# Optimization experiments

Measured on AMD Instinct MI355X. Metric: run time of the kernel, lower is better.

Reference implementation:

```python
import jax, jax.numpy as jnp
import numpy as np

# WAGE-style quantizer (NeuroSim training path): round to 2^(b-1) levels, clip to (-1+1/S, 1-1/S),
# straight-through estimator for gradients.

def wage_q(x, bits=8):
    S = 2.0 ** (bits - 1)
    q = jnp.clip(jnp.round(x * S) / S, -1.0 + 1.0 / S, 1.0 - 1.0 / S)
    return x + jax.lax.stop_gradient(q - x)


def qconv(x, w, stride, pad, wl_w=8, wl_a=8):
    wq = wage_q(w, wl_w)
    y = jax.lax.conv_general_dilated(
        x, wq, window_strides=(stride, stride),
        padding=[(pad, pad), (pad, pad)],
        dimension_numbers=('NCHW', 'OIHW', 'NCHW'))
    return wage_q(y, wl_a)


def pad_hw(x, p):
    return jnp.pad(x, ((0, 0), (0, 0), (p, p), (p, p)))


def crop_like(x, tgt):
    return x[:, :, :tgt.shape[2], :tgt.shape[3]]


WEIGHT_SHAPES = {
    'w1': (64, 4, 3, 3), 'w2': (128, 64, 3, 3), 'w3': (256, 128, 3, 3), 'w4': (512, 256, 3, 3),
    'wr11': (512, 512, 3, 3), 'wr12': (512, 512, 3, 3), 'wr21': (512, 512, 3, 3), 'wr22': (512, 512, 3, 3),
    'wd3': (128, 512, 4, 4), 'wd2': (64, 416, 4, 4), 'wd1': (4, 224, 4, 4),
    'wu43': (32, 512, 4, 4), 'wu32': (32, 416, 4, 4), 'wu21': (32, 224, 4, 4), 'wu10': (32, 100, 4, 4),
    'wfc': (1, 32),
}


def setup_inputs() -> dict:
    key = jax.random.key(0)
    keys = jax.random.split(key, len(WEIGHT_SHAPES) + 1)
    inp = {'x': jax.random.normal(keys[0], (8, 4, 256, 256), dtype=jnp.float32)}
    for i, (name, shp) in enumerate(WEIGHT_SHAPES.items()):
        fan_in = int(np.prod(shp[1:]))
        inp[name] = jax.random.normal(keys[i + 1], shp, dtype=jnp.float32) / np.sqrt(fan_in)
    return inp


def reference(x, w1, w2, w3, w4, wr11, wr12, wr21, wr22,
              wd3, wd2, wd1, wu43, wu32, wu21, wu10, wfc):
    c1 = qconv(x, w1, 2, 1)        # [B,64,128,128]
    c2 = qconv(c1, w2, 2, 1)       # [B,128,64,64]
    c3 = qconv(c2, w3, 2, 1)       # [B,256,32,32]
    c4 = qconv(c3, w4, 2, 1)       # [B,512,16,16]
    r11 = qconv(c4, wr11, 1, 1)
    r12 = (1.0 - qconv(r11, wr12, 1, 1)) * c4
    r21 = qconv(r12, wr21, 1, 1)
    r22 = (1.0 - qconv(r21, wr22, 1, 1)) * r12
    r22p = pad_hw(r22, 8)                                   # [B,512,32,32]
    flow4_up = crop_like(qconv(r22p, wu43, 1, 2), c3)       # [B,32,32,32]
    d3 = crop_like(qconv(r22p, wd3, 1, 2), c3)              # [B,128,32,32]
    cat3 = pad_hw(jnp.concatenate([c3, d3, flow4_up], 1), 16)  # [B,416,64,64]
    flow3_up = crop_like(qconv(cat3, wu32, 1, 2), c2)
    d2 = crop_like(qconv(cat3, wd2, 1, 2), c2)
    cat2 = pad_hw(jnp.concatenate([c2, d2, flow3_up], 1), 32)  # [B,224,128,128]
    flow2_up = crop_like(qconv(cat2, wu21, 1, 2), c1)
    d1 = crop_like(qconv(cat2, wd1, 1, 2), c1)
    cat1 = pad_hw(jnp.concatenate([c1, d1, flow2_up], 1), 64)  # [B,100,256,256]
    u10 = qconv(cat1, wu10, 1, 2)                              # [B,32,257,257]
    feat = jnp.max(u10, axis=(2, 3))                           # AdaptiveMaxPool2d((1,1))
    out = wage_q(feat @ wage_q(wfc, 8).T, 8)                   # QLinear 32->1
    return out
```

## Files before the change

kernel.cpp:

```cpp
#include <hip/hip_runtime.h>

#define DEV __device__ __forceinline__

typedef __attribute__((ext_vector_type(4))) int i32x4;

DEV int wqi(float y) {
    int q = (int)rintf(y * 128.0f);
    return q < -127 ? -127 : (q > 127 ? 127 : q);
}
DEV unsigned encf(float f) { unsigned u = __float_as_uint(f); return (u & 0x80000000u) ? ~u : (u | 0x80000000u); }
DEV float decf(unsigned u) { return (u & 0x80000000u) ? __uint_as_float(u ^ 0x80000000u) : __uint_as_float(~u); }
DEV float wq8f(float x) {
    float q = rintf(x * 128.0f) * 0.0078125f;
    return fminf(fmaxf(q, -0.9921875f), 0.9921875f);
}

#define GLOAD16(g, l) __builtin_amdgcn_global_load_lds( \
    (const __attribute__((address_space(1))) void*)(g), \
    (__attribute__((address_space(3))) void*)(l), 16, 0, 0)

struct PackDesc {
    const float* w0; const float* w1; uint4* dst;
    int OC0, OC1, CinW, K, noct, nch64u, ndup;
};
struct PackArgs { PackDesc d[11]; int bofs[12]; };

__global__ void __launch_bounds__(256) k_packall(PackArgs a) {
    __shared__ unsigned char sb[16 * (64 * 16 + 4)];
    const int b = blockIdx.x;
    int i = 0;
    #pragma unroll
    for (int j = 1; j < 11; ++j) if (b >= a.bofs[j]) i = j;
    const PackDesc D = a.d[i];
    const int b2 = b - a.bofs[i];
    const int oct = b2 % D.noct;
    const int ch64u = b2 / D.noct;
    const int K2 = D.K * D.K;
    const int row_elems = 64 * K2;
    const int SSTR = row_elems + 4;
    const int QR = row_elems / 4;
    const int NQ = 16 * QR;
    const int cin0 = ch64u * 64;
    const int tid = threadIdx.x;

    for (int q = tid; q < NQ; q += 256) {
        const int r = q / QR, j = q - r * QR;
        const int oc = oct * 16 + r;
        const float* src = nullptr; int oci = 0;
        if (oc < D.OC0) { src = D.w0; oci = oc; }
        else if (oc < D.OC0 + D.OC1) { src = D.w1; oci = oc - D.OC0; }
        const int e0 = j * 4;
        float v[4] = {0.f, 0.f, 0.f, 0.f};
        if (src != nullptr) {
            const float* p = src + ((size_t)oci * D.CinW + cin0) * K2 + e0;
            const int cin_last = cin0 + (e0 + 3) / K2;
            if (cin_last < D.CinW) {
                const float4 f4 = *(const float4*)p;
                v[0] = f4.x; v[1] = f4.y; v[2] = f4.z; v[3] = f4.w;
            } else {
                #pragma unroll
                for (int e = 0; e < 4; ++e) {
                    const int cin = cin0 + (e0 + e) / K2;
                    if (cin < D.CinW) v[e] = p[e];
                }
            }
        }
        unsigned pk = 0;
        #pragma unroll
        for (int e = 0; e < 4; ++e) pk |= ((unsigned)(wqi(v[e]) & 255)) << (e * 8);
        *(unsigned*)&sb[r * SSTR + e0] = pk;
    }
    __syncthreads();

    const int outN = K2 * 64;
    for (int idx = tid; idx < outN; idx += 256) {
        const int kpos = idx >> 6, lane = idx & 63;
        const int l15 = lane & 15, g = lane >> 4;
        unsigned wd[4] = {0u, 0u, 0u, 0u};
        #pragma unroll
        for (int e = 0; e < 16; ++e) {
            const unsigned bval = sb[l15 * SSTR + (g * 16 + e) * K2 + kpos];
            wd[e >> 2] |= bval << ((e & 3) * 8);
        }
        uint4 u; u.x = wd[0]; u.y = wd[1]; u.z = wd[2]; u.w = wd[3];
        for (int d = 0; d < D.ndup; ++d) {
            const int ch64 = ch64u + d * D.nch64u;
            D.dst[((size_t)(ch64 * K2 + kpos) * D.noct + oct) * 64 + lane] = u;
        }
    }
}

__global__ void __launch_bounds__(256) k_conv1(const float* __restrict__ x, const float* __restrict__ w1,
                                               signed char* __restrict__ cat1) {
    __shared__ float sw2[36][64];
    __shared__ float sin_[4][17][17];
    const int tid = threadIdx.x;
    const int n = blockIdx.y;
    const int oh0 = (blockIdx.x >> 4) * 8, ow0 = (blockIdx.x & 15) * 8;
    for (int i = tid; i < 2304; i += 256) sw2[i % 36][i / 36] = wq8f(w1[i]);
    const int ih0 = oh0 * 2 - 1, iw0 = ow0 * 2 - 1;
    for (int i = tid; i < 4 * 289; i += 256) {
        const int c = i / 289, rem = i % 289, r = rem / 17, cc = rem % 17;
        const int ih = ih0 + r, iw = iw0 + cc;
        float v = 0.f;
        if ((unsigned)ih < 256u && (unsigned)iw < 256u) v = x[((size_t)(n * 4 + c) * 256 + ih) * 256 + iw];
        sin_[c][r][cc] = v;
    }
    __syncthreads();
    const int sp = tid & 63, ocg = tid >> 6;
    const int oh = sp >> 3, ow = sp & 7;
    float acc[16];
    #pragma unroll
    for (int j = 0; j < 16; ++j) acc[j] = 0.f;
    #pragma unroll
    for (int c = 0; c < 4; ++c)
    #pragma unroll
    for (int kh = 0; kh < 3; ++kh)
    #pragma unroll
    for (int kw = 0; kw < 3; ++kw) {
        const float v = sin_[c][oh * 2 + kh][ow * 2 + kw];
        const float4* wp4 = (const float4*)&sw2[c * 9 + kh * 3 + kw][ocg * 16];
        #pragma unroll
        for (int q = 0; q < 4; ++q) {
            const float4 wv = wp4[q];
            acc[q * 4 + 0] = fmaf(v, wv.x, acc[q * 4 + 0]);
            acc[q * 4 + 1] = fmaf(v, wv.y, acc[q * 4 + 1]);
            acc[q * 4 + 2] = fmaf(v, wv.z, acc[q * 4 + 2]);
            acc[q * 4 + 3] = fmaf(v, wv.w, acc[q * 4 + 3]);
        }
    }
    const size_t pix = ((size_t)(n * 128) + oh0 + oh) * 128 + ow0 + ow;
    unsigned wd[4] = {0u, 0u, 0u, 0u};
    #pragma unroll
    for (int j = 0; j < 16; ++j)
        wd[j >> 2] |= ((unsigned)(wqi(acc[j]) & 255)) << ((j & 3) * 8);
    uint4 u; u.x = wd[0]; u.y = wd[1]; u.z = wd[2]; u.w = wd[3];
    *(uint4*)(cat1 + pix * 112 + ocg * 16) = u;
}

__global__ void k_init(unsigned* __restrict__ feat, uint4* __restrict__ zbuf) {
    feat[threadIdx.x] = encf(-2.0f);
    if (threadIdx.x < 64) { uint4 z; z.x = z.y = z.z = z.w = 0u; zbuf[threadIdx.x] = z; }
}

__global__ void k_fc(const unsigned* __restrict__ feat, const float* __restrict__ wfc,
                     float* __restrict__ out) {
    int n = threadIdx.x;
    if (n < 8) {
        float s = 0.f;
        for (int c = 0; c < 32; ++c) s += decf(feat[n * 32 + c]) * wq8f(wfc[c]);
        out[n] = wq8f(s);
    }
}

__global__ void __launch_bounds__(256) k_comb(const int* __restrict__ ps, int nsl, int radix,
                                              int NP, int OC, double inv,
                                              signed char* __restrict__ dst, int dstr, int dch) {
    const int t = blockIdx.x * 256 + threadIdx.x;
    const int total = NP * (OC / 4);
    if (t >= total) return;
    const int opc = OC / 4;
    const int pix = t / opc, oc0 = (t - pix * opc) * 4;
    const size_t base = (size_t)pix * OC + oc0;
    const size_t NPOC = (size_t)NP * OC;
    long v0 = 0, v1 = 0, v2 = 0, v3 = 0;
    for (int s = 0; s < nsl; ++s) {
        const int4 p = *(const int4*)(ps + s * NPOC + base);
        v0 = v0 * radix + p.x; v1 = v1 * radix + p.y;
        v2 = v2 * radix + p.z; v3 = v3 * radix + p.w;
    }
    unsigned pk = 0;
    pk |= (unsigned)(wqi((float)((double)v0 * inv)) & 255);
    pk |= (unsigned)(wqi((float)((double)v1 * inv)) & 255) << 8;
    pk |= (unsigned)(wqi((float)((double)v2 * inv)) & 255) << 16;
    pk |= (unsigned)(wqi((float)((double)v3 * inv)) & 255) << 24;
    *(unsigned*)(dst + (size_t)pix * dstr + dch + oc0) = pk;
}

template<int K, int STR, int WM, int WN, int BN, int NBUF, int MODE, int RESF, int NSLICE, int NCHPS>
__global__ void __launch_bounds__(256) k_mconv(
    const signed char* __restrict__ s0, int Ctot, int st0,
    int S, int padeff,
    const uint4* __restrict__ wqp, int noct,
    signed char* __restrict__ dst, int dstr, int dch,
    signed char* __restrict__ dhl, int dhlstr, short* __restrict__ dj,
    const void* __restrict__ res, int rstr,
    unsigned* __restrict__ feat, int* __restrict__ ps,
    const signed char* __restrict__ zbuf,
    int OCv, int OH, int OW, int TILES_W, int nch,
    int NT, int NOCG, int swzq, int ORD)
{
    constexpr int TH = WM * 4;
    constexpr int RH = (TH - 1) * STR + K, RW = 7 * STR + K;
    constexpr int UPPS = 5;
    constexpr int K2 = K * K;
    constexpr int NUS = RH * RW * UPPS;
    constexpr int ROUNDS = (NUS + 255) / 256;
    constexpr int NUPS = ROUNDS * 256;
    constexpr int AHEAD = NBUF - 1;
    __shared__ uint4 lds[NBUF * NUPS];
    __shared__ float sred[4][2][16];

    const int tid = threadIdx.x, lane = tid & 63, w = tid >> 6;
    const int wm = w % WM, wn = w / WM;
    const int l15 = lane & 15, g = lane >> 4;

    const int b = blockIdx.x;
    const int work = (b & 7) * swzq + (b >> 3);
    int tile, n, ocg, slice;
    if (ORD == 0) {
        ocg = work % NOCG; const int t2 = work / NOCG;
        tile = t2 % NT; const int t3 = t2 / NT;
        n = t3 & 7; slice = t3 >> 3;
    } else {
        tile = work % NT; const int t2 = work / NT;
        n = t2 & 7; const int t3 = t2 >> 3;
        ocg = t3 % NOCG; slice = t3 / NOCG;
    }
    const int cin_off = slice * nch * 64;
    const uint4* wqpS = wqp + (size_t)slice * nch * K2 * noct * 64;

    const int tileh = tile / TILES_W, tilew = tile % TILES_W;
    const int oh0 = tileh * TH, ow0 = tilew * 8;
    const int ih0 = oh0 * STR - padeff, iw0 = ow0 * STR - padeff;
    const int blk_oct0 = ocg * (WN * BN);

    int pixb[2];
    #pragma unroll
    for (int am = 0; am < 2; ++am) {
        const int sp = wm * 32 + am * 16 + l15;
        pixb[am] = ((sp >> 3) * STR) * RW + (sp & 7) * STR;
    }

    i32x4 acc[2][BN];
    #pragma unroll
    for (int am = 0; am < 2; ++am)
        #pragma unroll
        for (int bn = 0; bn < BN; ++bn) acc[am][bn] = (i32x4){0, 0, 0, 0};
    long acc64[(NSLICE > 1) ? 2 * BN * 4 : 1];
    #pragma unroll
    for (int q = 0; q < ((NSLICE > 1) ? 2 * BN * 4 : 1); ++q) acc64[q] = 0;

    auto issue = [&](int ch, int buf) {
        uint4* lb = &lds[buf * NUPS];
        #pragma unroll
        for (int rd = 0; rd < ROUNDS; ++rd) {
            const int d = rd * 256 + tid;
            const signed char* gp = zbuf;
            if (d < NUS) {
                const int pix = d / UPPS;
                const int u = d - pix * UPPS;
                const int r = pix / RW, c = pix - r * RW;
                const int ih = ih0 + r, iw = iw0 + c;
                const int cin = cin_off + ch * 64 + u * 16;
                if (u < 4 && (unsigned)ih < (unsigned)S && (unsigned)iw < (unsigned)S && cin < Ctot)
                    gp = s0 + (((size_t)n * S + ih) * S + iw) * st0 + cin;
            }
            GLOAD16(gp, lb + rd * 256 + (tid & ~63));
        }
    };

    #pragma unroll
    for (int i = 0; i < AHEAD; ++i) if (i < nch) issue(i, i % NBUF);

    for (int ch = 0; ch < nch; ++ch) {
        if (ch + AHEAD < nch) issue(ch + AHEAD, (ch + AHEAD) % NBUF);
        const int infl = (nch - 1 - ch < AHEAD) ? nch - 1 - ch : AHEAD;
        if (infl >= 2)      __builtin_amdgcn_s_waitcnt(0xF70 | (2 * ROUNDS));
        else if (infl == 1) __builtin_amdgcn_s_waitcnt(0xF70 | ROUNDS);
        else                __builtin_amdgcn_s_waitcnt(0xF70);
        __builtin_amdgcn_s_barrier();
        __builtin_amdgcn_sched_barrier(0);
        const int bufo = (ch % NBUF) * NUPS;
        const int pb0 = bufo + pixb[0] * UPPS + g;
        const int pb1 = bufo + pixb[1] * UPPS + g;
        const size_t wbase = ((size_t)ch * K2 * noct + blk_oct0 + wn * BN) * 64 + lane;
        #pragma unroll
        for (int kpos = 0; kpos < K2; ++kpos) {
            const int kh = kpos / K, kw = kpos % K;
            const int po = (kh * RW + kw) * UPPS;
            i32x4 bfr[BN];
            #pragma unroll
            for (int bn = 0; bn < BN; ++bn) {
                union { uint4 u; i32x4 v; } bu;
                bu.u = wqpS[wbase + ((size_t)kpos * noct + bn) * 64];
                bfr[bn] = bu.v;
            }
            union { uint4 u; i32x4 v; } a0, a1;
            a0.u = lds[pb0 + po];
            a1.u = lds[pb1 + po];
            #pragma unroll
            for (int bn = 0; bn < BN; ++bn) {
                acc[0][bn] = __builtin_amdgcn_mfma_i32_16x16x64_i8(a0.v, bfr[bn], acc[0][bn], 0, 0, 0);
                acc[1][bn] = __builtin_amdgcn_mfma_i32_16x16x64_i8(a1.v, bfr[bn], acc[1][bn], 0, 0, 0);
            }
        }
        if constexpr (NSLICE > 1) {
            if (((ch + 1) & (NCHPS - 1)) == 0) {
                #pragma unroll
                for (int am = 0; am < 2; ++am)
                #pragma unroll
                for (int bn = 0; bn < BN; ++bn) {
                    #pragma unroll
                    for (int rg = 0; rg < 4; ++rg) {
                        acc64[(am * BN + bn) * 4 + rg] = acc64[(am * BN + bn) * 4 + rg] * 256 + (long)acc[am][bn][rg];
                    }
                    acc[am][bn] = (i32x4){0, 0, 0, 0};
                }
            }
        }
        __builtin_amdgcn_sched_barrier(0);
        __builtin_amdgcn_s_barrier();
    }

    if constexpr (MODE == 2) {
        #pragma unroll
        for (int bn = 0; bn < BN; ++bn) {
            float m = -2.0f;
            #pragma unroll
            for (int am = 0; am < 2; ++am)
                #pragma unroll
                for (int rg = 0; rg < 4; ++rg) {
                    const int sp = wm * 32 + am * 16 + g * 4 + rg;
                    const int oh = oh0 + (sp >> 3), ow = ow0 + (sp & 7);
                    float v = -2.0f;
                    if (oh < OH && ow < OW) {
                        const float y = (float)acc[am][bn][rg] * (1.f / 16384.f);
                        v = (float)wqi(y) * 0.0078125f;
                    }
                    m = fmaxf(m, v);
                }
            m = fmaxf(m, __shfl_xor(m, 16));
            m = fmaxf(m, __shfl_xor(m, 32));
            if (lane < 16) sred[w][bn][l15] = m;
        }
        __syncthreads();
        if (tid < BN * 16) {
            const int bn = tid >> 4, l = tid & 15;
            float mm = sred[0][bn][l];
            #pragma unroll
            for (int i = 1; i < WM * WN; ++i) mm = fmaxf(mm, sred[i][bn][l]);
            atomicMax(&feat[n * 32 + (blk_oct0 + bn) * 16 + l], encf(mm));
        }
    } else if constexpr (MODE == 3) {
        #pragma unroll
        for (int am = 0; am < 2; ++am)
        #pragma unroll
        for (int bn = 0; bn < BN; ++bn)
        #pragma unroll
        for (int rg = 0; rg < 4; ++rg) {
            const int sp = wm * 32 + am * 16 + g * 4 + rg;
            const int oh = oh0 + (sp >> 3), ow = ow0 + (sp & 7);
            const int oc = (blk_oct0 + wn * BN + bn) * 16 + l15;
            if (oh < OH && ow < OW && oc < OCv) {
                ps[(((size_t)slice * 8 + n) * OH * OW + (size_t)oh * OW + ow) * OCv + oc] = acc[am][bn][rg];
            }
        }
    } else {
        #pragma unroll
        for (int am = 0; am < 2; ++am)
        #pragma unroll
        for (int bn = 0; bn < BN; ++bn)
        #pragma unroll
        for (int rg = 0; rg < 4; ++rg) {
            const int sp = wm * 32 + am * 16 + g * 4 + rg;
            const int oh = oh0 + (sp >> 3), ow = ow0 + (sp & 7);
            const int oc = (blk_oct0 + wn * BN + bn) * 16 + l15;
            if (oh < OH && ow < OW && oc < OCv) {
                const size_t pixo = (size_t)(n * OH + oh) * OW + ow;
                float y;
                if constexpr (NSLICE == 1)      y = (float)acc[am][bn][rg] * (1.f / 16384.f);
                else if constexpr (NSLICE == 2) y = (float)((double)acc64[(am * BN + bn) * 4 + rg] * (1.0 / 2097152.0));
                else                            y = (float)((double)acc64[(am * BN + bn) * 4 + rg] * (1.0 / 268435456.0));
                const int qi = wqi(y);
                if constexpr (MODE == 0) {
                    dst[pixo * dstr + dch + oc] = (signed char)qi;
                } else {
                    const int rvi = (RESF == 1) ? (int)((const signed char*)res)[pixo * rstr + oc]
                                                : (int)((const short*)res)[pixo * rstr + oc];
                    const int j = (128 - qi) * rvi;
                    const int d0 = ((j + 128) & 255) - 128;
                    const int t1 = (j - d0) >> 8;
                    if constexpr (RESF == 1) {
                        dhl[pixo * dhlstr + oc] = (signed char)t1;
                        dhl[pixo * dhlstr + 512 + oc] = (signed char)d0;
                        dj[pixo * 512 + oc] = (short)j;
                    } else {
                        const int d1 = ((t1 + 128) & 255) - 128;
                        const int d2 = (t1 - d1) >> 8;
                        dhl[pixo * dhlstr + oc] = (signed char)d2;
                        dhl[pixo * dhlstr + 512 + oc] = (signed char)d1;
                        dhl[pixo * dhlstr + 1024 + oc] = (signed char)d0;
                    }
                }
            }
        }
    }
}

extern "C" void kernel_launch(void* const* d_in, const int* in_sizes, int n_in,
                              void* d_out, int out_size, void* d_ws, size_t ws_size,
                              hipStream_t stream)
{
    (void)in_sizes; (void)n_in; (void)out_size; (void)ws_size;
    const float* x = (const float*)d_in[0];
    const float* wfc = (const float*)d_in[16];
    float* out = (float*)d_out;

    char* ws = (char*)d_ws;
    size_t off = 0;
    auto alloc = [&](size_t bytes) { char* p = ws + off; off += (bytes + 255) & ~(size_t)255; return p; };

    struct PH { int i0, OC0, i1, OC1, CinW, K, noct, nch64u, ndup; };
    static const PH ph[11] = {
        {2, 128, -1, 0,  64, 3,  8, 1, 1},
        {3, 256, -1, 0, 128, 3, 16, 2, 1},
        {4, 512, -1, 0, 256, 3, 32, 4, 1},
        {5, 512, -1, 0, 512, 3, 32, 8, 1},
        {6, 512, -1, 0, 512, 3, 32, 8, 1},
        {7, 512, -1, 0, 512, 3, 32, 8, 2},
        {8, 512, -1, 0, 512, 3, 32, 8, 1},
        {9, 128, 12, 32, 512, 4, 10, 8, 3},
        {10, 64, 13, 32, 416, 4,  6, 7, 1},
        {11,  4, 14, 32, 224, 4,  3, 4, 1},
        {15, 32, -1, 0, 100, 4,  2, 2, 1}};

    PackArgs pa;
    int bacc = 0;
    uint4* wp[11];
    for (int i = 0; i < 11; ++i) {
        const int nch64 = ph[i].nch64u * ph[i].ndup;
        const int nel = nch64 * ph[i].K * ph[i].K * ph[i].noct * 64;
        wp[i] = (uint4*)alloc((size_t)nel * 16);
        pa.d[i].w0 = (const float*)d_in[ph[i].i0];
        pa.d[i].w1 = (ph[i].i1 >= 0) ? (const float*)d_in[ph[i].i1] : nullptr;
        pa.d[i].dst = wp[i];
        pa.d[i].OC0 = ph[i].OC0; pa.d[i].OC1 = ph[i].OC1;
        pa.d[i].CinW = ph[i].CinW; pa.d[i].K = ph[i].K; pa.d[i].noct = ph[i].noct;
        pa.d[i].nch64u = ph[i].nch64u; pa.d[i].ndup = ph[i].ndup;
        pa.bofs[i] = bacc;
        bacc += ph[i].noct * ph[i].nch64u;
    }
    pa.bofs[11] = bacc;

    signed char* cat1b = (signed char*)alloc((size_t)8*128*128*112);
    signed char* cat2b = (signed char*)alloc((size_t)8*64*64*224);
    signed char* cat3b = (signed char*)alloc((size_t)8*32*32*416);
    signed char* c4b   = (signed char*)alloc((size_t)8*16*16*512);
    signed char* r11b  = (signed char*)alloc((size_t)8*16*16*512);
    signed char* r12d  = (signed char*)alloc((size_t)8*16*16*1024);
    short*       r12j  = (short*)alloc((size_t)8*16*16*512 * 2);
    signed char* r22d  = (signed char*)alloc((size_t)8*16*16*1536);
    int*         psum  = (int*)alloc((size_t)3*8*32*32*160 * 4);
    unsigned*    featb = (unsigned*)alloc(256 * 4);
    uint4*       zbuf  = (uint4*)alloc(1024);

    k_packall<<<dim3((unsigned)bacc), dim3(256), 0, stream>>>(pa);
    k_init<<<dim3(1), dim3(256), 0, stream>>>(featb, zbuf);
    k_conv1<<<dim3(256, 8), dim3(256), 0, stream>>>(x, (const float*)d_in[1], cat1b);

    const signed char* zb = (const signed char*)zbuf;

    k_mconv<3,2,2,2,2,1,0,0,1,1><<<dim3(1024), 256, 0, stream>>>(
        cat1b,64,112, 128,1, wp[0],8, cat2b,224,0, nullptr,0,nullptr, nullptr,0, nullptr,nullptr, zb,
        128,64,64,8, 1, 64,2,128, 0);
    k_mconv<3,2,2,2,2,2,0,0,1,1><<<dim3(512), 256, 0, stream>>>(
        cat2b,128,224, 64,1, wp[1],16, cat3b,416,0, nullptr,0,nullptr, nullptr,0, nullptr,nullptr, zb,
        256,32,32,4, 2, 16,4,64, 0);
    k_mconv<3,2,2,2,1,2,3,0,1,1><<<dim3(1024), 256, 0, stream>>>(
        cat3b,256,416, 32,1, wp[2],32, nullptr,0,0, nullptr,0,nullptr, nullptr,0, nullptr,psum, zb,
        512,16,16,2, 2, 4,16,128, 1);
    k_comb<<<dim3(1024), 256, 0, stream>>>(psum, 2, 1, 2048, 512, 1.0/16384.0, c4b, 512, 0);
    k_mconv<3,1,2,2,1,3,3,0,1,1><<<dim3(1024), 256, 0, stream>>>(
        c4b,512,512, 16,1, wp[3],32, nullptr,0,0, nullptr,0,nullptr, nullptr,0, nullptr,psum, zb,
        512,16,16,2, 4, 4,16,128, 1);
    k_comb<<<dim3(1024), 256, 0, stream>>>(psum, 2, 1, 2048, 512, 1.0/16384.0, r11b, 512, 0);
    k_mconv<3,1,2,2,1,3,1,1,1,1><<<dim3(512), 256, 0, stream>>>(
        r11b,512,512, 16,1, wp[4],32, nullptr,0,0, r12d,1024,r12j, c4b,512, nullptr,nullptr, zb,
        512,16,16,2, 8, 4,16,64, 1);
    k_mconv<3,1,2,2,1,3,3,0,1,1><<<dim3(1024), 256, 0, stream>>>(
        r12d,1024,1024, 16,1, wp[5],32, nullptr,0,0, nullptr,0,nullptr, nullptr,0, nullptr,psum, zb,
        512,16,16,2, 8, 4,16,128, 1);
    k_comb<<<dim3(1024), 256, 0, stream>>>(psum, 2, 256, 2048, 512, 1.0/2097152.0, r11b, 512, 0);
    k_mconv<3,1,2,2,1,3,1,2,1,1><<<dim3(512), 256, 0, stream>>>(
        r11b,512,512, 16,1, wp[6],32, nullptr,0,0, r22d,1536,nullptr, r12j,512, nullptr,nullptr, zb,
        512,16,16,2, 8, 4,16,64, 1);
    k_mconv<4,1,2,2,1,3,3,0,1,1><<<dim3(1920), 256, 0, stream>>>(
        r22d,1536,1536, 16,10, wp[7],10, nullptr,0,0, nullptr,0,nullptr, nullptr,0, nullptr,psum, zb,
        160,32,32,4, 8, 16,5,240, 1);
    k_comb<<<dim3(1280), 256, 0, stream>>>(psum, 3, 256, 8192, 160, 1.0/268435456.0, cat3b, 416, 256);
    k_mconv<4,1,4,1,2,2,0,0,1,1><<<dim3(768), 256, 0, stream>>>(
        cat3b,416,416, 32,18, wp[8],6, cat2b,224,128, nullptr,0,nullptr, nullptr,0, nullptr,nullptr, zb,
        96,64,64,8, 7, 32,3,96, 0);
    k_mconv<4,1,4,1,3,2,0,0,1,1><<<dim3(1024), 256, 0, stream>>>(
        cat2b,224,224, 64,34, wp[9],3, cat1b,112,64, nullptr,0,nullptr, nullptr,0, nullptr,nullptr, zb,
        48,128,128,16, 4, 128,1,128, 0);
    k_mconv<4,1,4,1,2,2,2,0,1,1><<<dim3(4488), 256, 0, stream>>>(
        cat1b,112,112, 128,66, wp[10],2, nullptr,0,0, nullptr,0,nullptr, nullptr,0, featb,nullptr, zb,
        32,257,257,33, 2, 561,1,561, 0);
    k_fc<<<dim3(1), dim3(64), 0, stream>>>(featb, wfc, out);
}
```

Baseline: 355.4 us.

## Move residual epilogue and slice combine into split-K reduction kernel

Measured after the change: 344.8 us. 3.0% less time.

```diff
diff --git a/kernel.cpp b/kernel.cpp
--- a/kernel.cpp
+++ b/kernel.cpp
@@ -153,38 +153,71 @@
     }
 }
 
-__global__ void __launch_bounds__(256) k_comb(const int* __restrict__ ps, int nsl, int radix,
+template<int CMODE>
+__global__ void __launch_bounds__(256) k_comb(const int* __restrict__ ps, int D, int G,
                                               int NP, int OC, double inv,
-                                              signed char* __restrict__ dst, int dstr, int dch) {
+                                              signed char* __restrict__ dst, int dstr, int dch,
+                                              const void* __restrict__ res, int rstr,
+                                              signed char* __restrict__ dhl, int dhlstr,
+                                              short* __restrict__ dj) {
     const int t = blockIdx.x * 256 + threadIdx.x;
-    const int total = NP * (OC / 4);
+    const int opc = OC / 4;
+    const int total = NP * opc;
     if (t >= total) return;
-    const int opc = OC / 4;
     const int pix = t / opc, oc0 = (t - pix * opc) * 4;
     const size_t base = (size_t)pix * OC + oc0;
     const size_t NPOC = (size_t)NP * OC;
-    long v0 = 0, v1 = 0, v2 = 0, v3 = 0;
-    for (int s = 0; s < nsl; ++s) {
-        const int4 p = *(const int4*)(ps + s * NPOC + base);
-        v0 = v0 * radix + p.x; v1 = v1 * radix + p.y;
-        v2 = v2 * radix + p.z; v3 = v3 * radix + p.w;
-    }
-    unsigned pk = 0;
-    pk |= (unsigned)(wqi((float)((double)v0 * inv)) & 255);
-    pk |= (unsigned)(wqi((float)((double)v1 * inv)) & 255) << 8;
-    pk |= (unsigned)(wqi((float)((double)v2 * inv)) & 255) << 16;
-    pk |= (unsigned)(wqi((float)((double)v3 * inv)) & 255) << 24;
-    *(unsigned*)(dst + (size_t)pix * dstr + dch + oc0) = pk;
-}
-
-template<int K, int STR, int WM, int WN, int BN, int NBUF, int MODE, int RESF, int NSLICE, int NCHPS>
+    long v[4] = {0, 0, 0, 0};
+    int sidx = 0;
+    for (int d = 0; d < D; ++d) {
+        long s0 = 0, s1 = 0, s2 = 0, s3 = 0;
+        for (int g = 0; g < G; ++g, ++sidx) {
+            const int4 p = *(const int4*)(ps + sidx * NPOC + base);
+            s0 += p.x; s1 += p.y; s2 += p.z; s3 += p.w;
+        }
+        v[0] = v[0] * 256 + s0; v[1] = v[1] * 256 + s1;
+        v[2] = v[2] * 256 + s2; v[3] = v[3] * 256 + s3;
+    }
+    if constexpr (CMODE == 0) {
+        unsigned pk = 0;
+        #pragma unroll
+        for (int j = 0; j < 4; ++j)
+            pk |= (unsigned)(wqi((float)((double)v[j] * inv)) & 255) << (j * 8);
+        *(unsigned*)(dst + (size_t)pix * dstr + dch + oc0) = pk;
+    } else {
+        #pragma unroll
+        for (int j = 0; j < 4; ++j) {
+            const int qi = wqi((float)((double)v[j] * inv));
+            const int oc = oc0 + j;
+            if constexpr (CMODE == 1) {
+                const int rv = (int)((const signed char*)res)[(size_t)pix * rstr + oc];
+                const int jj = (128 - qi) * rv;
+                const int d0 = ((jj + 128) & 255) - 128;
+                const int t1 = (jj - d0) >> 8;
+                dhl[(size_t)pix * dhlstr + oc] = (signed char)t1;
+                dhl[(size_t)pix * dhlstr + 512 + oc] = (signed char)d0;
+                dj[(size_t)pix * 512 + oc] = (short)jj;
+            } else {
+                const int rv = (int)((const short*)res)[(size_t)pix * rstr + oc];
+                const int jj = (128 - qi) * rv;
+                const int d0 = ((jj + 128) & 255) - 128;
+                const int t1 = (jj - d0) >> 8;
+                const int d1 = ((t1 + 128) & 255) - 128;
+                const int d2 = (t1 - d1) >> 8;
+                dhl[(size_t)pix * dhlstr + oc] = (signed char)d2;
+                dhl[(size_t)pix * dhlstr + 512 + oc] = (signed char)d1;
+                dhl[(size_t)pix * dhlstr + 1024 + oc] = (signed char)d0;
+            }
+        }
+    }
+}
+
+template<int K, int STR, int WM, int WN, int BN, int NBUF, int MODE>
 __global__ void __launch_bounds__(256) k_mconv(
     const signed char* __restrict__ s0, int Ctot, int st0,
     int S, int padeff,
     const uint4* __restrict__ wqp, int noct,
     signed char* __restrict__ dst, int dstr, int dch,
-    signed char* __restrict__ dhl, int dhlstr, short* __restrict__ dj,
-    const void* __restrict__ res, int rstr,
     unsigned* __restrict__ feat, int* __restrict__ ps,
     const signed char* __restrict__ zbuf,
     int OCv, int OH, int OW, int TILES_W, int nch,
@@ -237,9 +270,6 @@
     for (int am = 0; am < 2; ++am)
         #pragma unroll
         for (int bn = 0; bn < BN; ++bn) acc[am][bn] = (i32x4){0, 0, 0, 0};
-    long acc64[(NSLICE > 1) ? 2 * BN * 4 : 1];
-    #pragma unroll
-    for (int q = 0; q < ((NSLICE > 1) ? 2 * BN * 4 : 1); ++q) acc64[q] = 0;
 
     auto issue = [&](int ch, int buf) {
         uint4* lb = &lds[buf * NUPS];
@@ -293,20 +323,6 @@
             for (int bn = 0; bn < BN; ++bn) {
                 acc[0][bn] = __builtin_amdgcn_mfma_i32_16x16x64_i8(a0.v, bfr[bn], acc[0][bn], 0, 0, 0);
                 acc[1][bn] = __builtin_amdgcn_mfma_i32_16x16x64_i8(a1.v, bfr[bn], acc[1][bn], 0, 0, 0);
-            }
-        }
-        if constexpr (NSLICE > 1) {
-            if (((ch + 1) & (NCHPS - 1)) == 0) {
-                #pragma unroll
-                for (int am = 0; am < 2; ++am)
-                #pragma unroll
-                for (int bn = 0; bn < BN; ++bn) {
-                    #pragma unroll
-                    for (int rg = 0; rg < 4; ++rg) {
-                        acc64[(am * BN + bn) * 4 + rg] = acc64[(am * BN + bn) * 4 + rg] * 256 + (long)acc[am][bn][rg];
-                    }
-                    acc[am][bn] = (i32x4){0, 0, 0, 0};
-                }
             }
         }
         __builtin_amdgcn_sched_barrier(0);
@@ -368,31 +384,8 @@
             const int oc = (blk_oct0 + wn * BN + bn) * 16 + l15;
             if (oh < OH && ow < OW && oc < OCv) {
                 const size_t pixo = (size_t)(n * OH + oh) * OW + ow;
-                float y;
-                if constexpr (NSLICE == 1)      y = (float)acc[am][bn][rg] * (1.f / 16384.f);
-                else if constexpr (NSLICE == 2) y = (float)((double)acc64[(am * BN + bn) * 4 + rg] * (1.0 / 2097152.0));
-                else                            y = (float)((double)acc64[(am * BN + bn) * 4 + rg] * (1.0 / 268435456.0));
-                const int qi = wqi(y);
-                if constexpr (MODE == 0) {
-                    dst[pixo * dstr + dch + oc] = (signed char)qi;
-                } else {
-                    const int rvi = (RESF == 1) ? (int)((const signed char*)res)[pixo * rstr + oc]
-                                                : (int)((const short*)res)[pixo * rstr + oc];
-                    const int j = (128 - qi) * rvi;
-                    const int d0 = ((j + 128) & 255) - 128;
-                    const int t1 = (j - d0) >> 8;
-                    if constexpr (RESF == 1) {
-                        dhl[pixo * dhlstr + oc] = (signed char)t1;
-                        dhl[pixo * dhlstr + 512 + oc] = (signed char)d0;
-                        dj[pixo * 512 + oc] = (short)j;
-                    } else {
-                        const int d1 = ((t1 + 128) & 255) - 128;
-                        const int d2 = (t1 - d1) >> 8;
-                        dhl[pixo * dhlstr + oc] = (signed char)d2;
-                        dhl[pixo * dhlstr + 512 + oc] = (signed char)d1;
-                        dhl[pixo * dhlstr + 1024 + oc] = (signed char)d0;
-                    }
-                }
+                const float y = (float)acc[am][bn][rg] * (1.f / 16384.f);
+                dst[pixo * dstr + dch + oc] = (signed char)wqi(y);
             }
         }
     }
@@ -451,7 +444,7 @@
     signed char* r12d  = (signed char*)alloc((size_t)8*16*16*1024);
     short*       r12j  = (short*)alloc((size_t)8*16*16*512 * 2);
     signed char* r22d  = (signed char*)alloc((size_t)8*16*16*1536);
-    int*         psum  = (int*)alloc((size_t)3*8*32*32*160 * 4);
+    int*         psum  = (int*)alloc((size_t)4*8*16*16*512 * 4);
     unsigned*    featb = (unsigned*)alloc(256 * 4);
     uint4*       zbuf  = (uint4*)alloc(1024);
 
@@ -460,43 +453,46 @@
     k_conv1<<<dim3(256, 8), dim3(256), 0, stream>>>(x, (const float*)d_in[1], cat1b);
 
     const signed char* zb = (const signed char*)zbuf;
-
-    k_mconv<3,2,2,2,2,1,0,0,1,1><<<dim3(1024), 256, 0, stream>>>(
-        cat1b,64,112, 128,1, wp[0],8, cat2b,224,0, nullptr,0,nullptr, nullptr,0, nullptr,nullptr, zb,
+    const void* nv = nullptr;
+
+    k_mconv<3,2,2,2,2,1,0><<<dim3(1024), 256, 0, stream>>>(
+        cat1b,64,112, 128,1, wp[0],8, cat2b,224,0, nullptr,nullptr, zb,
         128,64,64,8, 1, 64,2,128, 0);
-    k_mconv<3,2,2,2,2,2,0,0,1,1><<<dim3(512), 256, 0, stream>>>(
-        cat2b,128,224, 64,1, wp[1],16, cat3b,416,0, nullptr,0,nullptr, nullptr,0, nullptr,nullptr, zb,
+    k_mconv<3,2,2,2,2,2,0><<<dim3(512), 256, 0, stream>>>(
+        cat2b,128,224, 64,1, wp[1],16, cat3b,416,0, nullptr,nullptr, zb,
         256,32,32,4, 2, 16,4,64, 0);
-    k_mconv<3,2,2,2,1,2,3,0,1,1><<<dim3(1024), 256, 0, stream>>>(
-        cat3b,256,416, 32,1, wp[2],32, nullptr,0,0, nullptr,0,nullptr, nullptr,0, nullptr,psum, zb,
-        512,16,16,2, 2, 4,16,128, 1);
-    k_comb<<<dim3(1024), 256, 0, stream>>>(psum, 2, 1, 2048, 512, 1.0/16384.0, c4b, 512, 0);
-    k_mconv<3,1,2,2,1,3,3,0,1,1><<<dim3(1024), 256, 0, stream>>>(
-        c4b,512,512, 16,1, wp[3],32, nullptr,0,0, nullptr,0,nullptr, nullptr,0, nullptr,psum, zb,
-        512,16,16,2, 4, 4,16,128, 1);
-    k_comb<<<dim3(1024), 256, 0, stream>>>(psum, 2, 1, 2048, 512, 1.0/16384.0, r11b, 512, 0);
-    k_mconv<3,1,2,2,1,3,1,1,1,1><<<dim3(512), 256, 0, stream>>>(
-        r11b,512,512, 16,1, wp[4],32, nullptr,0,0, r12d,1024,r12j, c4b,512, nullptr,nullptr, zb,
-        512,16,16,2, 8, 4,16,64, 1);
-    k_mconv<3,1,2,2,1,3,3,0,1,1><<<dim3(1024), 256, 0, stream>>>(
-        r12d,1024,1024, 16,1, wp[5],32, nullptr,0,0, nullptr,0,nullptr, nullptr,0, nullptr,psum, zb,
-        512,16,16,2, 8, 4,16,128, 1);
-    k_comb<<<dim3(1024), 256, 0, stream>>>(psum, 2, 256, 2048, 512, 1.0/2097152.0, r11b, 512, 0);
-    k_mconv<3,1,2,2,1,3,1,2,1,1><<<dim3(512), 256, 0, stream>>>(
-        r11b,512,512, 16,1, wp[6],32, nullptr,0,0, r22d,1536,nullptr, r12j,512, nullptr,nullptr, zb,
-        512,16,16,2, 8, 4,16,64, 1);
-    k_mconv<4,1,2,2,1,3,3,0,1,1><<<dim3(1920), 256, 0, stream>>>(
-        r22d,1536,1536, 16,10, wp[7],10, nullptr,0,0, nullptr,0,nullptr, nullptr,0, nullptr,psum, zb,
-        160,32,32,4, 8, 16,5,240, 1);
-    k_comb<<<dim3(1280), 256, 0, stream>>>(psum, 3, 256, 8192, 160, 1.0/268435456.0, cat3b, 416, 256);
-    k_mconv<4,1,4,1,2,2,0,0,1,1><<<dim3(768), 256, 0, stream>>>(
-        cat3b,416,416, 32,18, wp[8],6, cat2b,224,128, nullptr,0,nullptr, nullptr,0, nullptr,nullptr, zb,
+    k_mconv<3,2,2,2,2,1,3><<<dim3(1024), 256, 0, stream>>>(
+        cat3b,256,416, 32,1, wp[2],32, nullptr,0,0, nullptr,(int*)psum, zb,
+        512,16,16,2, 1, 4,8,128, 1);
+    k_comb<0><<<dim3(1024), 256, 0, stream>>>(psum,1,4, 2048,512, 1.0/16384.0, c4b,512,0, nv,0, nullptr,0,nullptr);
+    k_mconv<3,1,4,1,2,2,3><<<dim3(1024), 256, 0, stream>>>(
+        c4b,512,512, 16,1, wp[3],32, nullptr,0,0, nullptr,psum, zb,
+        512,16,16,2, 2, 2,16,128, 1);
+    k_comb<0><<<dim3(1024), 256, 0, stream>>>(psum,1,4, 2048,512, 1.0/16384.0, r11b,512,0, nv,0, nullptr,0,nullptr);
+    k_mconv<3,1,4,1,2,3,3><<<dim3(512), 256, 0, stream>>>(
+        r11b,512,512, 16,1, wp[4],32, nullptr,0,0, nullptr,psum, zb,
+        512,16,16,2, 4, 2,16,64, 1);
+    k_comb<1><<<dim3(1024), 256, 0, stream>>>(psum,1,2, 2048,512, 1.0/16384.0, nullptr,0,0, c4b,512, r12d,1024,r12j);
+    k_mconv<3,1,4,1,2,2,3><<<dim3(1024), 256, 0, stream>>>(
+        r12d,1024,1024, 16,1, wp[5],32, nullptr,0,0, nullptr,psum, zb,
+        512,16,16,2, 4, 2,16,128, 1);
+    k_comb<0><<<dim3(1024), 256, 0, stream>>>(psum,2,2, 2048,512, 1.0/2097152.0, r11b,512,0, nv,0, nullptr,0,nullptr);
+    k_mconv<3,1,4,1,2,3,3><<<dim3(512), 256, 0, stream>>>(
+        r11b,512,512, 16,1, wp[6],32, nullptr,0,0, nullptr,psum, zb,
+        512,16,16,2, 4, 2,16,64, 1);
+    k_comb<2><<<dim3(1024), 256, 0, stream>>>(psum,1,2, 2048,512, 1.0/16384.0, nullptr,0,0, r12j,512, r22d,1536,nullptr);
+    k_mconv<4,1,4,1,2,2,3><<<dim3(960), 256, 0, stream>>>(
+        r22d,1536,1536, 16,10, wp[7],10, nullptr,0,0, nullptr,psum, zb,
+        160,32,32,4, 8, 8,5,120, 1);
+    k_comb<0><<<dim3(1280), 256, 0, stream>>>(psum,3,1, 8192,160, 1.0/268435456.0, cat3b,416,256, nv,0, nullptr,0,nullptr);
+    k_mconv<4,1,4,1,2,2,0><<<dim3(768), 256, 0, stream>>>(
+        cat3b,416,416, 32,18, wp[8],6, cat2b,224,128, nullptr,nullptr, zb,
         96,64,64,8, 7, 32,3,96, 0);
-    k_mconv<4,1,4,1,3,2,0,0,1,1><<<dim3(1024), 256, 0, stream>>>(
-        cat2b,224,224, 64,34, wp[9],3, cat1b,112,64, nullptr,0,nullptr, nullptr,0, nullptr,nullptr, zb,
+    k_mconv<4,1,4,1,3,2,0><<<dim3(1024), 256, 0, stream>>>(
+        cat2b,224,224, 64,34, wp[9],3, cat1b,112,64, nullptr,nullptr, zb,
         48,128,128,16, 4, 128,1,128, 0);
-    k_mconv<4,1,4,1,2,2,2,0,1,1><<<dim3(4488), 256, 0, stream>>>(
-        cat1b,112,112, 128,66, wp[10],2, nullptr,0,0, nullptr,0,nullptr, nullptr,0, featb,nullptr, zb,
+    k_mconv<4,1,4,1,2,2,2><<<dim3(4488), 256, 0, stream>>>(
+        cat1b,112,112, 128,66, wp[10],2, nullptr,0,0, featb,nullptr, zb,
         32,257,257,33, 2, 561,1,561, 0);
     k_fc<<<dim3(1), dim3(64), 0, stream>>>(featb, wfc, out);
 }
```
